# Performance work log

Measured on AMD Instinct MI355X. Metric: run time of the kernel, lower is better.

The kernel has to match this reference:

```python
import jax, jax.numpy as jnp
import numpy as np

N_NODES = 50000
N_EDGES = 800000
IN_CH = 128
HID = 128
NUM_CLASSES = 10
NUM_GRAPHS = 64


def _linear_params(key, fan_in, fan_out):
    kw, kb = jax.random.split(key)
    s = 1.0 / np.sqrt(fan_in)
    W = jax.random.uniform(kw, (fan_in, fan_out), jnp.float32, -s, s)
    b = jax.random.uniform(kb, (fan_out,), jnp.float32, -s, s)
    return W, b


def setup_inputs() -> dict:
    key = jax.random.key(0)
    ks = jax.random.split(key, 16)
    x = jax.random.normal(ks[0], (N_NODES, IN_CH), jnp.float32)
    edge_index = jax.random.randint(ks[1], (2, N_EDGES), 0, N_NODES, jnp.int64)
    batch = jnp.sort(jax.random.randint(ks[2], (N_NODES,), 0, NUM_GRAPHS, jnp.int64))
    inp = {"x": x, "edge_index": edge_index, "batch": batch}
    # conv layer 1 (in -> hid)
    inp["Wk1"], inp["bk1"] = _linear_params(ks[3], IN_CH, HID)
    inp["Wq1"], inp["bq1"] = _linear_params(ks[4], IN_CH, HID)
    inp["Wv1"], inp["bv1"] = _linear_params(ks[5], IN_CH, HID)
    inp["Ws1"], inp["bs1"] = _linear_params(ks[6], IN_CH, HID)
    inp["b1"] = jnp.zeros((HID,), jnp.float32)
    # conv layer 2 (hid -> hid)
    inp["Wk2"], inp["bk2"] = _linear_params(ks[7], HID, HID)
    inp["Wq2"], inp["bq2"] = _linear_params(ks[8], HID, HID)
    inp["Wv2"], inp["bv2"] = _linear_params(ks[9], HID, HID)
    inp["Ws2"], inp["bs2"] = _linear_params(ks[10], HID, HID)
    inp["b2"] = jnp.zeros((HID,), jnp.float32)
    # final fc
    inp["fcW"], inp["fcb"] = _linear_params(ks[11], HID, NUM_CLASSES)
    return inp


def _res_gated_conv(x, src, dst, Wk, bk, Wq, bq, Wv, bv, Ws, bs, b):
    # k from target node i, q and v from source node j (PyG ResGatedGraphConv)
    k = x @ Wk + bk            # [N, H]
    q = x @ Wq + bq            # [N, H]
    v = x @ Wv + bv            # [N, H]
    gate = jax.nn.sigmoid(k[dst] + q[src])   # [E, H]
    msg = gate * v[src]                       # [E, H]
    agg = jax.ops.segment_sum(msg, dst, num_segments=x.shape[0])
    return agg + x @ Ws + bs + b


def _global_mean_pool(x, batch, num_graphs):
    sums = jax.ops.segment_sum(x, batch, num_segments=num_graphs)
    cnts = jax.ops.segment_sum(jnp.ones((x.shape[0],), x.dtype), batch, num_segments=num_graphs)
    return sums / jnp.maximum(cnts, 1.0)[:, None]


def reference(x, edge_index, batch,
              Wk1, bk1, Wq1, bq1, Wv1, bv1, Ws1, bs1, b1,
              Wk2, bk2, Wq2, bq2, Wv2, bv2, Ws2, bs2, b2,
              fcW, fcb):
    src, dst = edge_index[0], edge_index[1]
    h = _res_gated_conv(x, src, dst, Wk1, bk1, Wq1, bq1, Wv1, bv1, Ws1, bs1, b1)
    h = jax.nn.relu(h)
    h = _res_gated_conv(h, src, dst, Wk2, bk2, Wq2, bq2, Wv2, bv2, Ws2, bs2, b2)
    h = jax.nn.relu(h)
    g = _global_mean_pool(h, batch, NUM_GRAPHS)   # [NUM_GRAPHS, HID]
    return g @ fcW + fcb                           # [NUM_GRAPHS, NUM_CLASSES]
```

## Files before the change

### kernel.cpp

```cpp
#include <hip/hip_runtime.h>
#include <math.h>


typedef __attribute__((ext_vector_type(8))) short short8;
typedef __attribute__((ext_vector_type(4))) float floatx4;
typedef __attribute__((ext_vector_type(8))) unsigned short ushort8v;

#define LOG2E 1.4426950408889634f
#define DSTRIDE 96

__device__ __forceinline__ unsigned short f2b(float f) {
  unsigned int u = __builtin_bit_cast(unsigned int, f);
  u += 0x7fff + ((u >> 16) & 1);
  return (unsigned short)(u >> 16);
}
__device__ __forceinline__ float blo(unsigned int u) {
  return __builtin_bit_cast(float, u << 16);
}
__device__ __forceinline__ float bhi(unsigned int u) {
  return __builtin_bit_cast(float, u & 0xffff0000u);
}


__global__ __launch_bounds__(256) void scatter_kernel(const int* __restrict__ src,
                                                      const int* __restrict__ dst,
                                                      int* __restrict__ cnt,
                                                      int* __restrict__ es, int E) {
  int e = blockIdx.x * 256 + threadIdx.x;
  if (e < E) {
    int i = dst[e];
    int p = atomicAdd(&cnt[i], 1);
    if (p < DSTRIDE) es[i * DSTRIDE + p] = src[e];
  }
}


__global__ __launch_bounds__(256) void prep_kernel(
    const float* __restrict__ Wk1, const float* __restrict__ Wq1,
    const float* __restrict__ Wv1, const float* __restrict__ Ws1,
    const float* __restrict__ Wk2, const float* __restrict__ Wq2,
    const float* __restrict__ Wv2, const float* __restrict__ Ws2,
    unsigned short* __restrict__ WT,
    const float* __restrict__ bk1, const float* __restrict__ bq1,
    const float* __restrict__ bv1, const float* __restrict__ bs1,
    const float* __restrict__ b1,
    const float* __restrict__ bk2, const float* __restrict__ bq2,
    const float* __restrict__ bv2, const float* __restrict__ bs2,
    const float* __restrict__ b2,
    float* __restrict__ bcat,
    int* __restrict__ cnt, int ncnt4, int nzerob) {
  int b = blockIdx.x;
  if (b < nzerob) {
    int i = b * 256 + threadIdx.x;
    if (i < ncnt4) ((int4*)cnt)[i] = make_int4(0, 0, 0, 0);
    return;
  }
  b -= nzerob;
  if (b < 512) {
    int idx = b * 256 + threadIdx.x;
    int layer = idx >> 16;
    int rem = idx & 0xFFFF;
    int mat = rem >> 14;
    int nk = rem & 0x3FFF;
    int nn = nk >> 7, kk = nk & 127;
    int sel = layer * 4 + mat;
    const float* W = (sel == 0) ? Wk1 : (sel == 1) ? Wq1 : (sel == 2) ? Wv1 :
                     (sel == 3) ? Ws1 : (sel == 4) ? Wk2 : (sel == 5) ? Wq2 :
                     (sel == 6) ? Wv2 : Ws2;
    WT[idx] = f2b(W[kk * 128 + nn]);
    return;
  }
  b -= 512;
  {
    int idx = b * 256 + threadIdx.x;
    if (idx >= 1024) return;
    int layer = idx >> 9;
    int rem = idx & 511;
    int mat = rem >> 7, c = rem & 127;
    int sel = layer * 4 + mat;
    const float* bb = (sel == 0) ? bk1 : (sel == 1) ? bq1 : (sel == 2) ? bv1 :
                      (sel == 3) ? bs1 : (sel == 4) ? bk2 : (sel == 5) ? bq2 :
                      (sel == 6) ? bv2 : bs2;
    float v = bb[c];
    if (mat == 3) v += (layer == 0) ? b1[c] : b2[c];
    bcat[idx] = v;
  }
}


__global__ __launch_bounds__(256) void gemm_mfma_kernel(
    const float* __restrict__ Xf, const unsigned short* __restrict__ Xb,
    int use_fp32,
    const unsigned short* __restrict__ WT,
    const float* __restrict__ bcat,
    unsigned short* __restrict__ Kb, unsigned short* __restrict__ QV,
    unsigned short* __restrict__ Sb, int n) {
  __shared__ unsigned short aT[128 * 136];
  __shared__ float estage_all[4][16 * 68];

  int t = threadIdx.x;
  int row0 = blockIdx.x * 128;

  if (use_fp32) {
#pragma unroll
    for (int i = 0; i < 8; ++i) {
      int c = i * 256 + t;
      int r = c >> 4, col16 = c & 15;
      ushort8v o;
#pragma unroll
      for (int q = 0; q < 8; ++q) o[q] = 0;
      if (row0 + r < n) {
        float4 u0 = *(const float4*)&Xf[(size_t)(row0 + r) * 128 + col16 * 8];
        float4 u1 = *(const float4*)&Xf[(size_t)(row0 + r) * 128 + col16 * 8 + 4];
        o[0] = f2b(u0.x); o[1] = f2b(u0.y); o[2] = f2b(u0.z); o[3] = f2b(u0.w);
        o[4] = f2b(u1.x); o[5] = f2b(u1.y); o[6] = f2b(u1.z); o[7] = f2b(u1.w);
      }
      *(ushort8v*)&aT[r * 136 + col16 * 8] = o;
    }
  } else {
#pragma unroll
    for (int i = 0; i < 8; ++i) {
      int c = i * 256 + t;
      int r = c >> 4, col16 = c & 15;
      int4 v = make_int4(0, 0, 0, 0);
      if (row0 + r < n) v = *(const int4*)&Xb[(size_t)(row0 + r) * 128 + col16 * 8];
      *(int4*)&aT[r * 136 + col16 * 8] = v;
    }
  }
  __syncthreads();

  int lane = t & 63, wid = t >> 6;
  int wy = wid >> 1, wx = wid & 1;
  int l15 = lane & 15, lq = lane >> 4;
  int r4 = lane >> 2, cq4 = lane & 3;
  int col = wx * 64 + cq4 * 16;
  float* estage = estage_all[wid];

#pragma unroll
  for (int mm = 0; mm < 2; ++mm) {
    int m = blockIdx.y * 2 + mm;
    const unsigned short* WTm = WT + (size_t)m * 16384;

    floatx4 acc[4][4];
#pragma unroll
    for (int mf = 0; mf < 4; ++mf)
#pragma unroll
      for (int nf = 0; nf < 4; ++nf) acc[mf][nf] = (floatx4)(0.0f);

#pragma unroll
    for (int ks = 0; ks < 4; ++ks) {
      int kof = ks * 32 + lq * 8;
      short8 a[4], b[4];
#pragma unroll
      for (int mf = 0; mf < 4; ++mf)
        a[mf] = *(const short8*)&aT[(wy * 64 + mf * 16 + l15) * 136 + kof];
#pragma unroll
      for (int nf = 0; nf < 4; ++nf)
        b[nf] = *(const short8*)&WTm[(size_t)(wx * 64 + nf * 16 + l15) * 128 + kof];
#pragma unroll
      for (int mf = 0; mf < 4; ++mf)
#pragma unroll
        for (int nf = 0; nf < 4; ++nf)
          acc[mf][nf] = __builtin_amdgcn_mfma_f32_16x16x32_bf16(a[mf], b[nf], acc[mf][nf], 0, 0, 0);
    }

    const float* bias = bcat + m * 128;
    float4 bv[4];
#pragma unroll
    for (int j = 0; j < 4; ++j) bv[j] = *(const float4*)&bias[col + j * 4];

    unsigned short* Ob;
    int ostr;
    if (m == 0)      { Ob = Kb;       ostr = 128; }
    else if (m == 1) { Ob = QV;       ostr = 256; }
    else if (m == 2) { Ob = QV + 128; ostr = 256; }
    else             { Ob = Sb;       ostr = 128; }

#pragma unroll
    for (int mf = 0; mf < 4; ++mf) {
#pragma unroll
      for (int nf = 0; nf < 4; ++nf)
#pragma unroll
        for (int i = 0; i < 4; ++i)
          estage[(lq * 4 + i) * 68 + nf * 16 + l15] = acc[mf][nf][i];
      int grow = row0 + wy * 64 + mf * 16 + r4;
      if (grow < n) {
        float4 p[4];
#pragma unroll
        for (int j = 0; j < 4; ++j) {
          float4 e = *(const float4*)&estage[r4 * 68 + cq4 * 16 + j * 4];
          p[j].x = e.x + bv[j].x; p[j].y = e.y + bv[j].y;
          p[j].z = e.z + bv[j].z; p[j].w = e.w + bv[j].w;
        }
        ushort8v o0, o1;
        o0[0] = f2b(p[0].x); o0[1] = f2b(p[0].y); o0[2] = f2b(p[0].z); o0[3] = f2b(p[0].w);
        o0[4] = f2b(p[1].x); o0[5] = f2b(p[1].y); o0[6] = f2b(p[1].z); o0[7] = f2b(p[1].w);
        o1[0] = f2b(p[2].x); o1[1] = f2b(p[2].y); o1[2] = f2b(p[2].z); o1[3] = f2b(p[2].w);
        o1[4] = f2b(p[3].x); o1[5] = f2b(p[3].y); o1[6] = f2b(p[3].z); o1[7] = f2b(p[3].w);
        *(ushort8v*)&Ob[(size_t)grow * ostr + col] = o0;
        *(ushort8v*)&Ob[(size_t)grow * ostr + col + 8] = o1;
      }
    }
  }
}


__global__ __launch_bounds__(256) void edge_agg_kernel(
    const unsigned short* __restrict__ Kb, const unsigned short* __restrict__ QV,
    const unsigned short* __restrict__ Sb, const int* __restrict__ cnt,
    const int* __restrict__ es, unsigned short* __restrict__ Hb, int n) {
  int wid = threadIdx.x >> 6;
  int lane = threadIdx.x & 63;
  int node = blockIdx.x * 4 + wid;
  if (node >= n) return;
  int slot = lane >> 4;
  int l16 = lane & 15;
  int chb = l16 * 8;

  uint4 kk = *(const uint4*)&Kb[(size_t)node * 128 + chb];
  float kc0 = blo(kk.x) * (-LOG2E), kc1 = bhi(kk.x) * (-LOG2E);
  float kc2 = blo(kk.y) * (-LOG2E), kc3 = bhi(kk.y) * (-LOG2E);
  float kc4 = blo(kk.z) * (-LOG2E), kc5 = bhi(kk.z) * (-LOG2E);
  float kc6 = blo(kk.w) * (-LOG2E), kc7 = bhi(kk.w) * (-LOG2E);

  float a0 = 0.f, a1 = 0.f, a2 = 0.f, a3 = 0.f;
  float a4 = 0.f, a5 = 0.f, a6 = 0.f, a7 = 0.f;

  int count = cnt[node];
  if (count > DSTRIDE) count = DSTRIDE;
  const int* row = es + (size_t)node * DSTRIDE;
  int e = slot;
  int j = (e < count) ? row[e] : -1;
  while (j >= 0) {
    int en = e + 4;
    int jn = (en < count) ? row[en] : -1;
    const unsigned short* qvrow = &QV[(size_t)j * 256 + chb];
    uint4 q8 = *(const uint4*)qvrow;
    uint4 v8 = *(const uint4*)(qvrow + 128);
    float ex;
    ex = __builtin_amdgcn_exp2f(fmaf(blo(q8.x), -LOG2E, kc0));
    a0 = fmaf(blo(v8.x), __builtin_amdgcn_rcpf(1.0f + ex), a0);
    ex = __builtin_amdgcn_exp2f(fmaf(bhi(q8.x), -LOG2E, kc1));
    a1 = fmaf(bhi(v8.x), __builtin_amdgcn_rcpf(1.0f + ex), a1);
    ex = __builtin_amdgcn_exp2f(fmaf(blo(q8.y), -LOG2E, kc2));
    a2 = fmaf(blo(v8.y), __builtin_amdgcn_rcpf(1.0f + ex), a2);
    ex = __builtin_amdgcn_exp2f(fmaf(bhi(q8.y), -LOG2E, kc3));
    a3 = fmaf(bhi(v8.y), __builtin_amdgcn_rcpf(1.0f + ex), a3);
    ex = __builtin_amdgcn_exp2f(fmaf(blo(q8.z), -LOG2E, kc4));
    a4 = fmaf(blo(v8.z), __builtin_amdgcn_rcpf(1.0f + ex), a4);
    ex = __builtin_amdgcn_exp2f(fmaf(bhi(q8.z), -LOG2E, kc5));
    a5 = fmaf(bhi(v8.z), __builtin_amdgcn_rcpf(1.0f + ex), a5);
    ex = __builtin_amdgcn_exp2f(fmaf(blo(q8.w), -LOG2E, kc6));
    a6 = fmaf(blo(v8.w), __builtin_amdgcn_rcpf(1.0f + ex), a6);
    ex = __builtin_amdgcn_exp2f(fmaf(bhi(q8.w), -LOG2E, kc7));
    a7 = fmaf(bhi(v8.w), __builtin_amdgcn_rcpf(1.0f + ex), a7);
    e = en; j = jn;
  }

  a0 += __shfl_xor(a0, 16); a0 += __shfl_xor(a0, 32);
  a1 += __shfl_xor(a1, 16); a1 += __shfl_xor(a1, 32);
  a2 += __shfl_xor(a2, 16); a2 += __shfl_xor(a2, 32);
  a3 += __shfl_xor(a3, 16); a3 += __shfl_xor(a3, 32);
  a4 += __shfl_xor(a4, 16); a4 += __shfl_xor(a4, 32);
  a5 += __shfl_xor(a5, 16); a5 += __shfl_xor(a5, 32);
  a6 += __shfl_xor(a6, 16); a6 += __shfl_xor(a6, 32);
  a7 += __shfl_xor(a7, 16); a7 += __shfl_xor(a7, 32);

  if (slot == 0) {
    uint4 sb = *(const uint4*)&Sb[(size_t)node * 128 + chb];
    float r0 = fmaxf(a0 + blo(sb.x), 0.f), r1 = fmaxf(a1 + bhi(sb.x), 0.f);
    float r2 = fmaxf(a2 + blo(sb.y), 0.f), r3 = fmaxf(a3 + bhi(sb.y), 0.f);
    float r4 = fmaxf(a4 + blo(sb.z), 0.f), r5 = fmaxf(a5 + bhi(sb.z), 0.f);
    float r6 = fmaxf(a6 + blo(sb.w), 0.f), r7 = fmaxf(a7 + bhi(sb.w), 0.f);
    ushort8v o;
    o[0] = f2b(r0); o[1] = f2b(r1); o[2] = f2b(r2); o[3] = f2b(r3);
    o[4] = f2b(r4); o[5] = f2b(r5); o[6] = f2b(r6); o[7] = f2b(r7);
    *(ushort8v*)&Hb[(size_t)node * 128 + chb] = o;
  }
}


__device__ __forceinline__ int lb_batch(const int* __restrict__ batch, int n, int key) {
  int lo = 0, hi = n;
  while (lo < hi) {
    int mid = (lo + hi) >> 1;
    if (batch[mid] < key) lo = mid + 1; else hi = mid;
  }
  return lo;
}

__global__ __launch_bounds__(256) void pool_sum_kernel(const unsigned short* __restrict__ Hb,
                                                       const int* __restrict__ batch,
                                                       float* __restrict__ partial, int n) {
  __shared__ float red[8 * 128];
  int g = blockIdx.x >> 4;
  int slice = blockIdx.x & 15;
  int t = threadIdx.x;
  int grp = t >> 5;
  int cq = t & 31;
  int s = lb_batch(batch, n, g), e = lb_batch(batch, n, g + 1);
  int cntn = e - s;
  int per = (cntn + 15) >> 4;
  int ss = s + slice * per;
  int ee = ss + per; if (ee > e) ee = e;

  float4 acc = make_float4(0.f, 0.f, 0.f, 0.f);
  for (int nd = ss + grp; nd < ee; nd += 8) {
    uint2 u = *(const uint2*)&Hb[(size_t)nd * 128 + cq * 4];
    acc.x += blo(u.x); acc.y += bhi(u.x);
    acc.z += blo(u.y); acc.w += bhi(u.y);
  }
  *(float4*)&red[grp * 128 + cq * 4] = acc;
  __syncthreads();
  if (t < 128) {
    float tot = 0.f;
#pragma unroll
    for (int g8 = 0; g8 < 8; ++g8) tot += red[g8 * 128 + t];
    partial[(size_t)slice * 8192 + g * 128 + t] = tot;
  }
}

__global__ __launch_bounds__(128) void fc_kernel(const float* __restrict__ partial,
                                                 const int* __restrict__ batch,
                                                 const float* __restrict__ fcW,
                                                 const float* __restrict__ fcb,
                                                 float* __restrict__ out, int n) {
  __shared__ float p[128];
  int g = blockIdx.x;
  int t = threadIdx.x;
  int cntn = lb_batch(batch, n, g + 1) - lb_batch(batch, n, g);
  float inv = 1.0f / (float)((cntn > 0) ? cntn : 1);
  float tot = 0.f;
#pragma unroll
  for (int s = 0; s < 16; ++s) tot += partial[(size_t)s * 8192 + g * 128 + t];
  p[t] = tot * inv;
  __syncthreads();
  if (t < 10) {
    float s = fcb[t];
    for (int c = 0; c < 128; ++c) s += p[c] * fcW[c * 10 + t];
    out[g * 10 + t] = s;
  }
}


extern "C" void kernel_launch(void* const* d_in, const int* in_sizes, int n_in,
                              void* d_out, int out_size, void* d_ws, size_t ws_size,
                              hipStream_t stream) {
  const float* x   = (const float*)d_in[0];
  const int* eidx  = (const int*)d_in[1];
  const int* batch = (const int*)d_in[2];
  const float* Wk1 = (const float*)d_in[3];  const float* bk1 = (const float*)d_in[4];
  const float* Wq1 = (const float*)d_in[5];  const float* bq1 = (const float*)d_in[6];
  const float* Wv1 = (const float*)d_in[7];  const float* bv1 = (const float*)d_in[8];
  const float* Ws1 = (const float*)d_in[9];  const float* bs1 = (const float*)d_in[10];
  const float* b1  = (const float*)d_in[11];
  const float* Wk2 = (const float*)d_in[12]; const float* bk2 = (const float*)d_in[13];
  const float* Wq2 = (const float*)d_in[14]; const float* bq2 = (const float*)d_in[15];
  const float* Wv2 = (const float*)d_in[16]; const float* bv2 = (const float*)d_in[17];
  const float* Ws2 = (const float*)d_in[18]; const float* bs2 = (const float*)d_in[19];
  const float* b2  = (const float*)d_in[20];
  const float* fcW = (const float*)d_in[21]; const float* fcb = (const float*)d_in[22];
  float* out = (float*)d_out;

  const int N = in_sizes[0] / 128;
  const int E = in_sizes[1] / 2;
  const int* src = eidx;
  const int* dst = eidx + E;

  char* w = (char*)d_ws;
  size_t off = 0;
  auto carve = [&](size_t bytes) -> void* {
    void* p = w + off;
    off += (bytes + 255) & ~size_t(255);
    return p;
  };
  const size_t featB16 = (size_t)N * 128 * 2;
  unsigned short* Kb = (unsigned short*)carve(featB16);
  unsigned short* QV = (unsigned short*)carve(featB16 * 2);
  unsigned short* Hb = (unsigned short*)carve(featB16);
  unsigned short* Sb = (unsigned short*)carve(featB16);
  unsigned short* WT = (unsigned short*)carve(2 * 4 * 128 * 128 * 2);
  float* bcat = (float*)carve(1024 * 4);
  int* cnt     = (int*)carve(((size_t)N + 4) * 4);
  int* es      = (int*)carve((size_t)N * DSTRIDE * 4);
  float* partial = (float*)carve((size_t)16 * 64 * 128 * 4);
  (void)ws_size; (void)n_in; (void)out_size;

  int ncnt4 = (N + 3) / 4;
  int nzerob = (ncnt4 + 255) / 256;
  prep_kernel<<<nzerob + 512 + 4, 256, 0, stream>>>(
      Wk1, Wq1, Wv1, Ws1, Wk2, Wq2, Wv2, Ws2, WT,
      bk1, bq1, bv1, bs1, b1, bk2, bq2, bv2, bs2, b2, bcat,
      cnt, ncnt4, nzerob);

  scatter_kernel<<<(E + 255) / 256, 256, 0, stream>>>(src, dst, cnt, es, E);

  dim3 ggrid((N + 127) / 128, 2);

  gemm_mfma_kernel<<<ggrid, 256, 0, stream>>>(x, nullptr, 1, WT, bcat,
                                              Kb, QV, Sb, N);
  edge_agg_kernel<<<(N + 3) / 4, 256, 0, stream>>>(Kb, QV, Sb, cnt, es, Hb, N);

  gemm_mfma_kernel<<<ggrid, 256, 0, stream>>>(nullptr, Hb, 0, WT + 65536,
                                              bcat + 512, Kb, QV, Sb, N);
  edge_agg_kernel<<<(N + 3) / 4, 256, 0, stream>>>(Kb, QV, Sb, cnt, es, Hb, N);

  pool_sum_kernel<<<1024, 256, 0, stream>>>(Hb, batch, partial, N);
  fc_kernel<<<64, 128, 0, stream>>>(partial, batch, fcW, fcb, out, N);
}
```

Baseline: 349.6 us.

## Fuse edge scatter into first GEMM launch and unroll edge aggregation loop

The standalone edge-scatter kernel is folded into the first GEMM launch as extra trailing blocks, with the 2D grid flattened to 1D, so the CSR-like bucketing runs alongside the layer-1 projections and one launch disappears. The edge aggregation loop now handles two neighbors per iteration with independent gathers, replacing the prefetch-chained single-edge loop, to expose more memory-level parallelism. Scatter blocks still reserve the GEMM kernel's large shared memory, which may limit how many of them can co-reside.

```diff
diff --git a/kernel.cpp b/kernel.cpp
--- a/kernel.cpp
+++ b/kernel.cpp
@@ -19,19 +19,6 @@
 }
 __device__ __forceinline__ float bhi(unsigned int u) {
   return __builtin_bit_cast(float, u & 0xffff0000u);
-}
-
-
-__global__ __launch_bounds__(256) void scatter_kernel(const int* __restrict__ src,
-                                                      const int* __restrict__ dst,
-                                                      int* __restrict__ cnt,
-                                                      int* __restrict__ es, int E) {
-  int e = blockIdx.x * 256 + threadIdx.x;
-  if (e < E) {
-    int i = dst[e];
-    int p = atomicAdd(&cnt[i], 1);
-    if (p < DSTRIDE) es[i * DSTRIDE + p] = src[e];
-  }
 }
 
 
@@ -94,12 +81,26 @@
     const unsigned short* __restrict__ WT,
     const float* __restrict__ bcat,
     unsigned short* __restrict__ Kb, unsigned short* __restrict__ QV,
-    unsigned short* __restrict__ Sb, int n) {
+    unsigned short* __restrict__ Sb, int n, int gemmBlocks,
+    const int* __restrict__ esrc, const int* __restrict__ edst,
+    int* __restrict__ cnt, int* __restrict__ es, int E) {
   __shared__ unsigned short aT[128 * 136];
   __shared__ float estage_all[4][16 * 68];
 
   int t = threadIdx.x;
-  int row0 = blockIdx.x * 128;
+
+  if (blockIdx.x >= gemmBlocks) {
+    int e = (blockIdx.x - gemmBlocks) * 256 + t;
+    if (e < E) {
+      int i = edst[e];
+      int p = atomicAdd(&cnt[i], 1);
+      if (p < DSTRIDE) es[i * DSTRIDE + p] = esrc[e];
+    }
+    return;
+  }
+
+  int row0 = (blockIdx.x >> 1) * 128;
+  int ysel = blockIdx.x & 1;
 
   if (use_fp32) {
 #pragma unroll
@@ -138,7 +139,7 @@
 
 #pragma unroll
   for (int mm = 0; mm < 2; ++mm) {
-    int m = blockIdx.y * 2 + mm;
+    int m = ysel * 2 + mm;
     const unsigned short* WTm = WT + (size_t)m * 16384;
 
     floatx4 acc[4][4];
@@ -230,13 +231,15 @@
   if (count > DSTRIDE) count = DSTRIDE;
   const int* row = es + (size_t)node * DSTRIDE;
   int e = slot;
-  int j = (e < count) ? row[e] : -1;
-  while (j >= 0) {
-    int en = e + 4;
-    int jn = (en < count) ? row[en] : -1;
-    const unsigned short* qvrow = &QV[(size_t)j * 256 + chb];
-    uint4 q8 = *(const uint4*)qvrow;
-    uint4 v8 = *(const uint4*)(qvrow + 128);
+  while (e + 4 < count) {
+    int j0 = row[e];
+    int j1 = row[e + 4];
+    const unsigned short* qv0 = &QV[(size_t)j0 * 256 + chb];
+    const unsigned short* qv1 = &QV[(size_t)j1 * 256 + chb];
+    uint4 q8 = *(const uint4*)qv0;
+    uint4 v8 = *(const uint4*)(qv0 + 128);
+    uint4 q9 = *(const uint4*)qv1;
+    uint4 v9 = *(const uint4*)(qv1 + 128);
     float ex;
     ex = __builtin_amdgcn_exp2f(fmaf(blo(q8.x), -LOG2E, kc0));
     a0 = fmaf(blo(v8.x), __builtin_amdgcn_rcpf(1.0f + ex), a0);
@@ -254,7 +257,46 @@
     a6 = fmaf(blo(v8.w), __builtin_amdgcn_rcpf(1.0f + ex), a6);
     ex = __builtin_amdgcn_exp2f(fmaf(bhi(q8.w), -LOG2E, kc7));
     a7 = fmaf(bhi(v8.w), __builtin_amdgcn_rcpf(1.0f + ex), a7);
-    e = en; j = jn;
+    ex = __builtin_amdgcn_exp2f(fmaf(blo(q9.x), -LOG2E, kc0));
+    a0 = fmaf(blo(v9.x), __builtin_amdgcn_rcpf(1.0f + ex), a0);
+    ex = __builtin_amdgcn_exp2f(fmaf(bhi(q9.x), -LOG2E, kc1));
+    a1 = fmaf(bhi(v9.x), __builtin_amdgcn_rcpf(1.0f + ex), a1);
+    ex = __builtin_amdgcn_exp2f(fmaf(blo(q9.y), -LOG2E, kc2));
+    a2 = fmaf(blo(v9.y), __builtin_amdgcn_rcpf(1.0f + ex), a2);
+    ex = __builtin_amdgcn_exp2f(fmaf(bhi(q9.y), -LOG2E, kc3));
+    a3 = fmaf(bhi(v9.y), __builtin_amdgcn_rcpf(1.0f + ex), a3);
+    ex = __builtin_amdgcn_exp2f(fmaf(blo(q9.z), -LOG2E, kc4));
+    a4 = fmaf(blo(v9.z), __builtin_amdgcn_rcpf(1.0f + ex), a4);
+    ex = __builtin_amdgcn_exp2f(fmaf(bhi(q9.z), -LOG2E, kc5));
+    a5 = fmaf(bhi(v9.z), __builtin_amdgcn_rcpf(1.0f + ex), a5);
+    ex = __builtin_amdgcn_exp2f(fmaf(blo(q9.w), -LOG2E, kc6));
+    a6 = fmaf(blo(v9.w), __builtin_amdgcn_rcpf(1.0f + ex), a6);
+    ex = __builtin_amdgcn_exp2f(fmaf(bhi(q9.w), -LOG2E, kc7));
+    a7 = fmaf(bhi(v9.w), __builtin_amdgcn_rcpf(1.0f + ex), a7);
+    e += 8;
+  }
+  if (e < count) {
+    int j0 = row[e];
+    const unsigned short* qv0 = &QV[(size_t)j0 * 256 + chb];
+    uint4 q8 = *(const uint4*)qv0;
+    uint4 v8 = *(const uint4*)(qv0 + 128);
+    float ex;
+    ex = __builtin_amdgcn_exp2f(fmaf(blo(q8.x), -LOG2E, kc0));
+    a0 = fmaf(blo(v8.x), __builtin_amdgcn_rcpf(1.0f + ex), a0);
+    ex = __builtin_amdgcn_exp2f(fmaf(bhi(q8.x), -LOG2E, kc1));
+    a1 = fmaf(bhi(v8.x), __builtin_amdgcn_rcpf(1.0f + ex), a1);
+    ex = __builtin_amdgcn_exp2f(fmaf(blo(q8.y), -LOG2E, kc2));
+    a2 = fmaf(blo(v8.y), __builtin_amdgcn_rcpf(1.0f + ex), a2);
+    ex = __builtin_amdgcn_exp2f(fmaf(bhi(q8.y), -LOG2E, kc3));
+    a3 = fmaf(bhi(v8.y), __builtin_amdgcn_rcpf(1.0f + ex), a3);
+    ex = __builtin_amdgcn_exp2f(fmaf(blo(q8.z), -LOG2E, kc4));
+    a4 = fmaf(blo(v8.z), __builtin_amdgcn_rcpf(1.0f + ex), a4);
+    ex = __builtin_amdgcn_exp2f(fmaf(bhi(q8.z), -LOG2E, kc5));
+    a5 = fmaf(bhi(v8.z), __builtin_amdgcn_rcpf(1.0f + ex), a5);
+    ex = __builtin_amdgcn_exp2f(fmaf(blo(q8.w), -LOG2E, kc6));
+    a6 = fmaf(blo(v8.w), __builtin_amdgcn_rcpf(1.0f + ex), a6);
+    ex = __builtin_amdgcn_exp2f(fmaf(bhi(q8.w), -LOG2E, kc7));
+    a7 = fmaf(bhi(v8.w), __builtin_amdgcn_rcpf(1.0f + ex), a7);
   }
 
   a0 += __shfl_xor(a0, 16); a0 += __shfl_xor(a0, 32);
@@ -393,16 +435,17 @@
       bk1, bq1, bv1, bs1, b1, bk2, bq2, bv2, bs2, b2, bcat,
       cnt, ncnt4, nzerob);
 
-  scatter_kernel<<<(E + 255) / 256, 256, 0, stream>>>(src, dst, cnt, es, E);
-
-  dim3 ggrid((N + 127) / 128, 2);
-
-  gemm_mfma_kernel<<<ggrid, 256, 0, stream>>>(x, nullptr, 1, WT, bcat,
-                                              Kb, QV, Sb, N);
+  int gemmBlocks = ((N + 127) / 128) * 2;
+  int scatterBlocks = (E + 255) / 256;
+
+  gemm_mfma_kernel<<<gemmBlocks + scatterBlocks, 256, 0, stream>>>(
+      x, nullptr, 1, WT, bcat, Kb, QV, Sb, N, gemmBlocks,
+      src, dst, cnt, es, E);
   edge_agg_kernel<<<(N + 3) / 4, 256, 0, stream>>>(Kb, QV, Sb, cnt, es, Hb, N);
 
-  gemm_mfma_kernel<<<ggrid, 256, 0, stream>>>(nullptr, Hb, 0, WT + 65536,
-                                              bcat + 512, Kb, QV, Sb, N);
+  gemm_mfma_kernel<<<gemmBlocks, 256, 0, stream>>>(
+      nullptr, Hb, 0, WT + 65536, bcat + 512, Kb, QV, Sb, N, gemmBlocks,
+      nullptr, nullptr, nullptr, nullptr, 0);
   edge_agg_kernel<<<(N + 3) / 4, 256, 0, stream>>>(Kb, QV, Sb, cnt, es, Hb, N);
 
   pool_sum_kernel<<<1024, 256, 0, stream>>>(Hb, batch, partial, N);
```

Measured after the change: 366.3 us. 4.8% more time.
